# Optimization experiments

Measured on AMD Instinct MI355X. Metric: run time of the kernel, lower is better.

## Reference

```python
import jax, jax.numpy as jnp
import numpy as np

DATA_MAX = 30.0
LOG_FACTOR = float(np.log(DATA_MAX + 1.0))
THRESHOLDS = np.array([0.1, 1.0, 2.0, 5.0, 8.0], dtype=np.float32)
HIGHS = np.array([1.0, 2.0, 5.0, 8.0, np.inf], dtype=np.float32)
LEVEL_WEIGHTS = np.array([0.1, 0.1, 0.2, 0.25, 0.35], dtype=np.float32)
TIME_WEIGHTS = np.array([0.0075, 0.02, 0.03, 0.04, 0.05, 0.06, 0.07, 0.08, 0.09, 0.1,
                         0.09, 0.08, 0.07, 0.06, 0.05, 0.04, 0.03, 0.02, 0.0075, 0.005],
                        dtype=np.float32)


def setup_inputs() -> dict:
    key = jax.random.key(0)
    k1, k2, k3 = jax.random.split(key, 3)
    shape = (2, 20, 480, 480)
    pred_norm = jax.random.uniform(k1, shape, dtype=jnp.float32)
    target_norm = jax.random.uniform(k2, shape, dtype=jnp.float32)
    mask = jax.random.uniform(k3, shape, dtype=jnp.float32)
    return {"pred_norm": pred_norm, "target_norm": target_norm, "mask": mask}


def _metscore(pred_norm, target_norm, mask):
    # de-normalize to physical space (mm)
    pred = jnp.clip(jnp.expm1(pred_norm * LOG_FACTOR), 0.0, None)
    target = jnp.clip(jnp.expm1(target_norm * LOG_FACTOR), 0.0, None)
    B, T, H, W = pred.shape
    N = B * H * W
    # flatten each timestep across batch+space: [T, N]
    p = jnp.transpose(pred, (1, 0, 2, 3)).reshape(T, N)
    t = jnp.transpose(target, (1, 0, 2, 3)).reshape(T, N)
    m = (jnp.transpose(mask, (1, 0, 2, 3)).reshape(T, N) > 0.5)
    mf = m.astype(p.dtype)

    thr = jnp.asarray(THRESHOLDS)
    highs = jnp.asarray(HIGHS)
    lw = jnp.asarray(LEVEL_WEIGHTS)

    # ---- per-timestep masked correlation (excluding double-zero pixels) ----
    dz = (p < thr[0]) & (t < thr[0])
    mc = (m & ~dz).astype(p.dtype)                       # [T,N]
    cnt = mc.sum(-1)                                      # [T]
    safe_cnt = jnp.maximum(cnt, 1.0)
    p_mean = (p * mc).sum(-1) / safe_cnt
    t_mean = (t * mc).sum(-1) / safe_cnt
    dp = (p - p_mean[:, None]) * mc
    dt = (t - t_mean[:, None]) * mc
    num = (dp * dt).sum(-1)
    den = jnp.sqrt((dp * dp).sum(-1) * (dt * dt).sum(-1))
    r_time = jnp.where(cnt > 0, jnp.clip(num / (den + 1e-6), -1.0, 1.0), 0.0)  # [T]

    # ---- threshold-bin membership [T, L, N] ----
    p_in = ((p[:, None, :] >= thr[None, :, None]) & (p[:, None, :] < highs[None, :, None])).astype(p.dtype)
    t_in = ((t[:, None, :] >= thr[None, :, None]) & (t[:, None, :] < highs[None, :, None])).astype(p.dtype)

    hits = jnp.einsum('tln,tln,tn->tl', p_in, t_in, mf)   # [T,L]
    p_tot = jnp.einsum('tln,tn->tl', p_in, mf)            # hits + false alarms
    t_tot = jnp.einsum('tln,tn->tl', t_in, mf)            # hits + misses
    ts_mat = hits / (p_tot + t_tot - hits + 1e-8)         # [T,L]

    diff = jnp.abs(p - t) * mf                            # [T,N]
    mae_num = jnp.einsum('tln,tn->tl', t_in, diff)
    mae_mat = jnp.where(t_tot > 0, mae_num / jnp.maximum(t_tot, 1.0), 0.0)  # [T,L]

    # ---- score combination ----
    term_corr = jnp.sqrt(jnp.exp(r_time - 1.0))           # [T]
    term_mae = jnp.sqrt(jnp.exp(-mae_mat / 100.0))        # [T,L]
    score_time = term_corr * (lw[None, :] * ts_mat * term_mae).sum(-1)  # [T]

    tw = jnp.asarray(TIME_WEIGHTS)
    if T == tw.shape[0]:
        w_time = tw
    elif T < tw.shape[0]:
        w_time = tw[:T] / tw[:T].sum()
    else:
        w_time = jnp.ones((T,), dtype=p.dtype) / T
    total = (score_time * w_time).sum()
    return total, score_time, r_time, ts_mat, mae_mat, ts_mat.mean(0), mae_mat.mean(0)


def reference(pred_norm, target_norm, mask):
    return _metscore(pred_norm, target_norm, mask)
```

## Files before the change

### kernel.cpp

```cpp
#include <hip/hip_runtime.h>
#include <math.h>

#define TS   20
#define NL   5
#define NS   26
#define GX   45
#define TPB  256
#define F4PT 5
#define HW4  57600

constexpr float C1 = (float)(0.09531017980432486 / 3.4339872044851463);
constexpr float C2 = (float)(0.69314718055994531 / 3.4339872044851463);
constexpr float C3 = (float)(1.09861228866810969 / 3.4339872044851463);
constexpr float C4 = (float)(1.79175946922805500 / 3.4339872044851463);
constexpr float C5 = (float)(2.19722457733621938 / 3.4339872044851463);

__device__ __forceinline__ float expm1_ln31(float x)
{
#if __has_builtin(__builtin_amdgcn_exp2f)
    return __builtin_amdgcn_exp2f(x * 4.9541963103868751f) - 1.0f;
#else
    return __expf(x * 3.4339872044851463f) - 1.0f;
#endif
}

__device__ __forceinline__ void px(float pn, float tn, float mn,
    unsigned& pP, unsigned& tP, unsigned& hP, int& cnt, float cum[NL],
    float& sp, float& st, float& spt, float& spp, float& stt)
{
    bool mok = mn > 0.5f;
    float pm = mok ? pn : -1.0f;
    float qm = mok ? tn : -1.0f;
    bool p1 = pm >= C1, p2 = pm >= C2, p3 = pm >= C3, p4 = pm >= C4, p5 = pm >= C5;
    bool q1 = qm >= C1, q2 = qm >= C2, q3 = qm >= C3, q4 = qm >= C4, q5 = qm >= C5;
    int lp = (int)p1 + (int)p2 + (int)p3 + (int)p4 + (int)p5;
    int lq = (int)q1 + (int)q2 + (int)q3 + (int)q4 + (int)q5;
    unsigned ohp = 1u << (5 * lp);
    pP += ohp;
    tP += 1u << (5 * lq);
    hP += (lp == lq) ? ohp : 0u;
    float p = expm1_ln31(pn);
    float q = expm1_ln31(tn);
    bool cond = (lp | lq) != 0;
    cnt += cond ? 1 : 0;
    float pz = cond ? p : 0.0f;
    float qz = cond ? q : 0.0f;
    sp += pz;  st += qz;
    spt = fmaf(pz, qz, spt);
    spp = fmaf(pz, pz, spp);
    stt = fmaf(qz, qz, stt);
    float ad = fabsf(p - q);
    cum[0] += q1 ? ad : 0.0f;
    cum[1] += q2 ? ad : 0.0f;
    cum[2] += q3 ? ad : 0.0f;
    cum[3] += q4 ? ad : 0.0f;
    cum[4] += q5 ? ad : 0.0f;
}

__global__ __launch_bounds__(TPB) void metscore_pass1(
    const float4* __restrict__ pred, const float4* __restrict__ targ,
    const float4* __restrict__ mask, float* __restrict__ sums )
{
    const int t = blockIdx.y;
    const int b = blockIdx.z;
    const size_t base = ((size_t)b * TS + t) * (size_t)HW4
                      + (size_t)blockIdx.x * (F4PT * TPB) + threadIdx.x;

    unsigned pP = 0u, tP = 0u, hP = 0u;
    int cnt = 0;
    float cum[NL] = {0, 0, 0, 0, 0};
    float sp = 0, st = 0, spt = 0, spp = 0, stt = 0;

    float4 pv = pred[base], tv = targ[base], mv = mask[base];
    #pragma unroll
    for (int j = 0; j < F4PT; ++j) {
        float4 npv, ntv, nmv;
        if (j + 1 < F4PT) {
            npv = pred[base + (j + 1) * TPB];
            ntv = targ[base + (j + 1) * TPB];
            nmv = mask[base + (j + 1) * TPB];
        }
        px(pv.x, tv.x, mv.x, pP, tP, hP, cnt, cum, sp, st, spt, spp, stt);
        px(pv.y, tv.y, mv.y, pP, tP, hP, cnt, cum, sp, st, spt, spp, stt);
        px(pv.z, tv.z, mv.z, pP, tP, hP, cnt, cum, sp, st, spt, spp, stt);
        px(pv.w, tv.w, mv.w, pP, tP, hP, cnt, cum, sp, st, spt, spp, stt);
        if (j + 1 < F4PT) { pv = npv; tv = ntv; mv = nmv; }
    }

    unsigned c16[8];
    #pragma unroll
    for (int k = 0; k < 8; ++k) c16[k] = 0u;
    #pragma unroll
    for (int l = 0; l < NL; ++l) {
        c16[l >> 1]        += ((hP >> (5 * (l + 1))) & 31u) << (16 * (l & 1));
        c16[(5 + l) >> 1]  += ((pP >> (5 * (l + 1))) & 31u) << (16 * ((5 + l) & 1));
        c16[(10 + l) >> 1] += ((tP >> (5 * (l + 1))) & 31u) << (16 * ((10 + l) & 1));
    }
    c16[7] += (unsigned)cnt << 16;

    float f[10] = {cum[0], cum[1], cum[2], cum[3], cum[4], sp, st, spt, spp, stt};
    #pragma unroll
    for (int k = 0; k < 8; ++k) {
        unsigned x = c16[k];
        x += __shfl_down(x, 32); x += __shfl_down(x, 16); x += __shfl_down(x, 8);
        x += __shfl_down(x, 4);  x += __shfl_down(x, 2);  x += __shfl_down(x, 1);
        c16[k] = x;
    }
    #pragma unroll
    for (int k = 0; k < 10; ++k) {
        float x = f[k];
        x += __shfl_down(x, 32); x += __shfl_down(x, 16); x += __shfl_down(x, 8);
        x += __shfl_down(x, 4);  x += __shfl_down(x, 2);  x += __shfl_down(x, 1);
        f[k] = x;
    }

    __shared__ unsigned ldsU[4][8];
    __shared__ float    ldsF[4][10];
    const int lane = threadIdx.x & 63;
    const int wv   = threadIdx.x >> 6;
    if (lane == 0) {
        #pragma unroll
        for (int k = 0; k < 8; ++k) ldsU[wv][k] = c16[k];
        #pragma unroll
        for (int k = 0; k < 10; ++k) ldsF[wv][k] = f[k];
    }
    __syncthreads();
    if (threadIdx.x < 8) {
        unsigned s = ldsU[0][threadIdx.x] + ldsU[1][threadIdx.x]
                   + ldsU[2][threadIdx.x] + ldsU[3][threadIdx.x];
        int c0 = 2 * threadIdx.x, c1 = c0 + 1;
        int n0 = (c0 == 15) ? 20 : c0;
        int n1 = (c1 == 15) ? 20 : c1;
        atomicAdd(&sums[t * NS + n0], (float)(s & 0xFFFFu));
        atomicAdd(&sums[t * NS + n1], (float)(s >> 16));
    } else if (threadIdx.x < 18) {
        int k = threadIdx.x - 8;
        float s = ldsF[0][k] + ldsF[1][k] + ldsF[2][k] + ldsF[3][k];
        int n = (k < 5) ? (15 + k) : (16 + k);
        atomicAdd(&sums[t * NS + n], s);
    }
}

__global__ __launch_bounds__(128) void metscore_final(
    const float* __restrict__ sums, float* __restrict__ out)
{
    __shared__ float ts_s[TS][NL];
    __shared__ float mae_s[TS][NL];
    __shared__ float sc_s[TS];
    const int tid = threadIdx.x;

    if (tid < TS * NL) {
        int tt_ = tid / NL, l = tid % NL;
        const float* s = sums + tt_ * NS;
        float h = s[l], pt = s[5 + l], tt = s[10 + l];
        float mn = s[15 + l] - ((l < NL - 1) ? s[16 + l] : 0.0f);
        float ts  = h / (pt + tt - h + 1e-8f);
        float mae = (tt > 0.0f) ? (mn / fmaxf(tt, 1.0f)) : 0.0f;
        ts_s[tt_][l]  = ts;
        mae_s[tt_][l] = mae;
        out[41 + tid]  = ts;
        out[141 + tid] = mae;
    }
    __syncthreads();

    if (tid < TS) {
        const float* s = sums + tid * NS;
        double cnt = s[20], sp = s[21], st = s[22];
        double spt = s[23], spp = s[24], stt = s[25];
        double sc = fmax(cnt, 1.0);
        double pmn = sp / sc, tmn = st / sc;
        double num = spt - pmn * st - tmn * sp + pmn * tmn * cnt;
        double vp  = spp - 2.0 * pmn * sp + pmn * pmn * cnt;
        double vt  = stt - 2.0 * tmn * st + tmn * tmn * cnt;
        double r = num / (sqrt(vp * vt) + 1e-6);
        r = fmin(fmax(r, -1.0), 1.0);
        float rt = (cnt > 0.0) ? (float)r : 0.0f;
        out[21 + tid] = rt;

        const float LW[NL] = {0.1f, 0.1f, 0.2f, 0.25f, 0.35f};
        float term_corr = sqrtf(expf(rt - 1.0f));
        float accl = 0.0f;
        #pragma unroll
        for (int l = 0; l < NL; ++l)
            accl += LW[l] * ts_s[tid][l] * sqrtf(expf(-mae_s[tid][l] * 0.01f));
        float sct = term_corr * accl;
        out[1 + tid] = sct;

        const float TW[TS] = {0.0075f, 0.02f, 0.03f, 0.04f, 0.05f, 0.06f, 0.07f,
                              0.08f, 0.09f, 0.1f, 0.09f, 0.08f, 0.07f, 0.06f,
                              0.05f, 0.04f, 0.03f, 0.02f, 0.0075f, 0.005f};
        sc_s[tid] = sct * TW[tid];
    }
    __syncthreads();

    if (tid == 0) {
        float tot = 0.0f;
        for (int k = 0; k < TS; ++k) tot += sc_s[k];
        out[0] = tot;
    }
    if (tid < NL) {
        float a = 0.0f, bsum = 0.0f;
        for (int k = 0; k < TS; ++k) { a += ts_s[k][tid]; bsum += mae_s[k][tid]; }
        out[241 + tid] = a * (1.0f / TS);
        out[246 + tid] = bsum * (1.0f / TS);
    }
}

extern "C" void kernel_launch(void* const* d_in, const int* in_sizes, int n_in,
                              void* d_out, int out_size, void* d_ws, size_t ws_size,
                              hipStream_t stream) {
    (void)in_sizes; (void)n_in; (void)out_size; (void)ws_size;
    const float4* pred = (const float4*)d_in[0];
    const float4* targ = (const float4*)d_in[1];
    const float4* mask = (const float4*)d_in[2];
    float* out  = (float*)d_out;
    float* sums = (float*)d_ws;

    hipMemsetAsync(sums, 0, TS * NS * sizeof(float), stream);

    dim3 grid(GX, TS, 2);
    metscore_pass1<<<grid, TPB, 0, stream>>>(pred, targ, mask, sums);
    metscore_final<<<1, 128, 0, stream>>>(sums, out);
}
```

Baseline: 138.9 us.

## Per-wave contiguous chunks with staged prefetch and derive count from hit bins

Each wave now reads its own contiguous chunk of float4s instead of striding across the block. Three tiles are loaded up front, the first is processed, then the rest are loaded, with sched_barriers pinning this order so memory latency is covered. The per-pixel count is dropped: the double-zero count comes from the level-0 hit field, and the final kernel subtracts it from the total pixel count. This saves a few ALU ops per pixel but hardcodes 460800 pixels per timestep and raises register pressure from holding five float4 triples.

```diff
diff --git a/kernel.cpp b/kernel.cpp
--- a/kernel.cpp
+++ b/kernel.cpp
@@ -8,6 +8,7 @@
 #define TPB  256
 #define F4PT 5
 #define HW4  57600
+#define WCH  (F4PT * 64)
 
 constexpr float C1 = (float)(0.09531017980432486 / 3.4339872044851463);
 constexpr float C2 = (float)(0.69314718055994531 / 3.4339872044851463);
@@ -25,7 +26,7 @@
 }
 
 __device__ __forceinline__ void px(float pn, float tn, float mn,
-    unsigned& pP, unsigned& tP, unsigned& hP, int& cnt, float cum[NL],
+    unsigned& pP, unsigned& tP, unsigned& hP, float cum[NL],
     float& sp, float& st, float& spt, float& spp, float& stt)
 {
     bool mok = mn > 0.5f;
@@ -35,16 +36,15 @@
     bool q1 = qm >= C1, q2 = qm >= C2, q3 = qm >= C3, q4 = qm >= C4, q5 = qm >= C5;
     int lp = (int)p1 + (int)p2 + (int)p3 + (int)p4 + (int)p5;
     int lq = (int)q1 + (int)q2 + (int)q3 + (int)q4 + (int)q5;
-    unsigned ohp = 1u << (5 * lp);
-    pP += ohp;
-    tP += 1u << (5 * lq);
-    hP += (lp == lq) ? ohp : 0u;
+    unsigned op = 1u << (5 * lp);
+    unsigned ot = 1u << (5 * lq);
+    unsigned h  = op & ot;
+    pP += op;  tP += ot;  hP += h;
     float p = expm1_ln31(pn);
     float q = expm1_ln31(tn);
-    bool cond = (lp | lq) != 0;
-    cnt += cond ? 1 : 0;
-    float pz = cond ? p : 0.0f;
-    float qz = cond ? q : 0.0f;
+    bool keep = (h & 1u) == 0u;
+    float pz = keep ? p : 0.0f;
+    float qz = keep ? q : 0.0f;
     sp += pz;  st += qz;
     spt = fmaf(pz, qz, spt);
     spp = fmaf(pz, pz, spp);
@@ -63,28 +63,44 @@
 {
     const int t = blockIdx.y;
     const int b = blockIdx.z;
+    const int lane = threadIdx.x & 63;
+    const int wv   = (blockIdx.x << 2) + (threadIdx.x >> 6);
     const size_t base = ((size_t)b * TS + t) * (size_t)HW4
-                      + (size_t)blockIdx.x * (F4PT * TPB) + threadIdx.x;
+                      + (size_t)wv * WCH + lane;
+
+    float4 pv[F4PT], tv[F4PT], mv[F4PT];
+    #pragma unroll
+    for (int j = 0; j < 3; ++j) {
+        pv[j] = pred[base + j * 64];
+        tv[j] = targ[base + j * 64];
+        mv[j] = mask[base + j * 64];
+    }
+    __builtin_amdgcn_sched_barrier(0);
 
     unsigned pP = 0u, tP = 0u, hP = 0u;
-    int cnt = 0;
     float cum[NL] = {0, 0, 0, 0, 0};
     float sp = 0, st = 0, spt = 0, spp = 0, stt = 0;
 
-    float4 pv = pred[base], tv = targ[base], mv = mask[base];
-    #pragma unroll
-    for (int j = 0; j < F4PT; ++j) {
-        float4 npv, ntv, nmv;
-        if (j + 1 < F4PT) {
-            npv = pred[base + (j + 1) * TPB];
-            ntv = targ[base + (j + 1) * TPB];
-            nmv = mask[base + (j + 1) * TPB];
-        }
-        px(pv.x, tv.x, mv.x, pP, tP, hP, cnt, cum, sp, st, spt, spp, stt);
-        px(pv.y, tv.y, mv.y, pP, tP, hP, cnt, cum, sp, st, spt, spp, stt);
-        px(pv.z, tv.z, mv.z, pP, tP, hP, cnt, cum, sp, st, spt, spp, stt);
-        px(pv.w, tv.w, mv.w, pP, tP, hP, cnt, cum, sp, st, spt, spp, stt);
-        if (j + 1 < F4PT) { pv = npv; tv = ntv; mv = nmv; }
+    px(pv[0].x, tv[0].x, mv[0].x, pP, tP, hP, cum, sp, st, spt, spp, stt);
+    px(pv[0].y, tv[0].y, mv[0].y, pP, tP, hP, cum, sp, st, spt, spp, stt);
+    px(pv[0].z, tv[0].z, mv[0].z, pP, tP, hP, cum, sp, st, spt, spp, stt);
+    px(pv[0].w, tv[0].w, mv[0].w, pP, tP, hP, cum, sp, st, spt, spp, stt);
+    __builtin_amdgcn_sched_barrier(0);
+
+    #pragma unroll
+    for (int j = 3; j < F4PT; ++j) {
+        pv[j] = pred[base + j * 64];
+        tv[j] = targ[base + j * 64];
+        mv[j] = mask[base + j * 64];
+    }
+    __builtin_amdgcn_sched_barrier(0);
+
+    #pragma unroll
+    for (int j = 1; j < F4PT; ++j) {
+        px(pv[j].x, tv[j].x, mv[j].x, pP, tP, hP, cum, sp, st, spt, spp, stt);
+        px(pv[j].y, tv[j].y, mv[j].y, pP, tP, hP, cum, sp, st, spt, spp, stt);
+        px(pv[j].z, tv[j].z, mv[j].z, pP, tP, hP, cum, sp, st, spt, spp, stt);
+        px(pv[j].w, tv[j].w, mv[j].w, pP, tP, hP, cum, sp, st, spt, spp, stt);
     }
 
     unsigned c16[8];
@@ -96,7 +112,7 @@
         c16[(5 + l) >> 1]  += ((pP >> (5 * (l + 1))) & 31u) << (16 * ((5 + l) & 1));
         c16[(10 + l) >> 1] += ((tP >> (5 * (l + 1))) & 31u) << (16 * ((10 + l) & 1));
     }
-    c16[7] += (unsigned)cnt << 16;
+    c16[7] += (hP & 31u) << 16;
 
     float f[10] = {cum[0], cum[1], cum[2], cum[3], cum[4], sp, st, spt, spp, stt};
     #pragma unroll
@@ -116,13 +132,12 @@
 
     __shared__ unsigned ldsU[4][8];
     __shared__ float    ldsF[4][10];
-    const int lane = threadIdx.x & 63;
-    const int wv   = threadIdx.x >> 6;
+    const int wvb = threadIdx.x >> 6;
     if (lane == 0) {
         #pragma unroll
-        for (int k = 0; k < 8; ++k) ldsU[wv][k] = c16[k];
+        for (int k = 0; k < 8; ++k) ldsU[wvb][k] = c16[k];
         #pragma unroll
-        for (int k = 0; k < 10; ++k) ldsF[wv][k] = f[k];
+        for (int k = 0; k < 10; ++k) ldsF[wvb][k] = f[k];
     }
     __syncthreads();
     if (threadIdx.x < 8) {
@@ -165,7 +180,8 @@
 
     if (tid < TS) {
         const float* s = sums + tid * NS;
-        double cnt = s[20], sp = s[21], st = s[22];
+        double cnt = 460800.0 - (double)s[20];
+        double sp = s[21], st = s[22];
         double spt = s[23], spp = s[24], stt = s[25];
         double sc = fmax(cnt, 1.0);
         double pmn = sp / sc, tmn = st / sc;
```

New measurement: 137.3 us. About the same (-1.2%).
